# Performance work log

Measured on AMD Instinct MI355X. Metric: run time of the kernel, lower is better.

Reference implementation:

```python
import jax, jax.numpy as jnp
import numpy as np

NUM_USERS = 100000
NUM_ITEMS = 50000
NUM_NODES = NUM_USERS + NUM_ITEMS
EMBED_DIM = 64
NUM_LAYERS = 3
NUM_EDGES = 1000000


def setup_inputs() -> dict:
    key = jax.random.key(0)
    k_edge, k_emb = jax.random.split(key)
    edge_index = jax.random.randint(k_edge, (2, NUM_EDGES), 0, NUM_NODES, dtype=jnp.int64)
    # xavier_uniform for Embedding weight [N, d]
    limit = float(np.sqrt(6.0 / (NUM_NODES + EMBED_DIM)))
    emb = jax.random.uniform(k_emb, (NUM_NODES, EMBED_DIM), minval=-limit, maxval=limit, dtype=jnp.float32)
    alpha = jnp.full((NUM_LAYERS + 1,), 0.25, dtype=jnp.float32)
    return {"edge_index": edge_index, "emb": emb, "alpha": alpha}


def _gcn_norm(edge_index, num_nodes, dtype):
    # gcn_norm with add_self_loops=False, edge_weight = ones
    src, dst = edge_index[0], edge_index[1]
    w = jnp.ones((src.shape[0],), dtype=dtype)
    deg = jax.ops.segment_sum(w, dst, num_segments=num_nodes)  # degree at target
    deg_inv_sqrt = jnp.where(deg > 0, jax.lax.rsqrt(jnp.maximum(deg, 1e-30)), 0.0)
    return deg_inv_sqrt[src] * deg_inv_sqrt[dst]  # [E]


def get_embedding(emb, alpha, edge_index):
    src, dst = edge_index[0], edge_index[1]
    norm = _gcn_norm(edge_index, NUM_NODES, emb.dtype)  # [E]
    x = emb
    out = x * alpha[0]
    for i in range(NUM_LAYERS):
        # gather -> scale by edge norm -> scatter-add at target nodes
        msgs = norm[:, None] * x[src]                      # [E, d]
        x = jax.ops.segment_sum(msgs, dst, num_segments=NUM_NODES)  # [N, d]
        out = out + x * alpha[i + 1]
    return out


def reference(edge_index, emb, alpha):
    out = get_embedding(emb, alpha, edge_index)  # [N, d]
    out_src = out[edge_index[0]]                 # [E, d]
    out_dst = out[edge_index[1]]                 # [E, d]
    return jnp.sum(out_src * out_dst, axis=-1)   # [E]
```

## Files before the change

kernel.cpp:

```cpp
#include <hip/hip_runtime.h>
#include <hip/hip_fp16.h>

#define DIM 64
#define PCHUNK 2048
#define BSH 9
#define BNODES (1 << BSH)

__device__ __forceinline__ float2 h2f(unsigned int u) {
    __half2 h = *reinterpret_cast<__half2*>(&u);
    return __half22float2(h);
}
__device__ __forceinline__ unsigned int f2h(float a, float b) {
    __half2 h = __floats2half2_rn(a, b);
    return *reinterpret_cast<unsigned int*>(&h);
}

__device__ __forceinline__ bool edges_are_i64(const unsigned int* w) {
    unsigned int acc = 0;
#pragma unroll
    for (int k = 0; k < 8; ++k) acc |= w[2 * k + 1];
    return acc == 0;
}
__device__ __forceinline__ int ld_edge(const void* raw, bool is64, size_t idx) {
    return is64 ? (int)((const long long*)raw)[idx] : ((const int*)raw)[idx];
}

__global__ void k_partition(const void* ei_raw, int E, int NB, int CAP,
                            int* __restrict__ bwcnt, uint2* __restrict__ pe) {
    __shared__ int cnt[512], lstart[512], gb[512], lofs[512], psum[256];
    __shared__ uint2 stage[PCHUNK];
    __shared__ int gpos[PCHUNK];
    bool is64 = edges_are_i64((const unsigned int*)ei_raw);
    int base = blockIdx.x * PCHUNK;
    int n = E - base; if (n > PCHUNK) n = PCHUNK;
    int t = threadIdx.x;
    for (int b = t; b < 512; b += 256) { cnt[b] = 0; lofs[b] = 0; }
    __syncthreads();
    int s[8], d[8];
#pragma unroll
    for (int r = 0; r < 8; ++r) {
        int i = r * 256 + t;
        if (i < n) {
            s[r] = ld_edge(ei_raw, is64, (size_t)base + i);
            d[r] = ld_edge(ei_raw, is64, (size_t)E + base + i);
            atomicAdd(&cnt[d[r] >> BSH], 1);
        }
    }
    __syncthreads();
    int a0 = cnt[2 * t], a1 = cnt[2 * t + 1];
    psum[t] = a0 + a1;
    __syncthreads();
    int v = psum[t];
    for (int o = 1; o < 256; o <<= 1) {
        int tv = (t >= o) ? psum[t - o] : 0;
        __syncthreads();
        psum[t] += tv;
        __syncthreads();
    }
    int excl = psum[t] - v;
    lstart[2 * t] = excl;
    lstart[2 * t + 1] = excl + a0;
    __syncthreads();
    for (int b = t; b < NB; b += 256)
        if (cnt[b] > 0) gb[b] = atomicAdd(&bwcnt[b], cnt[b]);
    __syncthreads();
#pragma unroll
    for (int r = 0; r < 8; ++r) {
        int i = r * 256 + t;
        if (i < n) {
            int b = d[r] >> BSH;
            int j = atomicAdd(&lofs[b], 1);
            int slot = lstart[b] + j;
            stage[slot] = make_uint2((unsigned)s[r], (unsigned)d[r]);
            int gj = gb[b] + j;
            gpos[slot] = (gj < CAP) ? (b * CAP + gj) : (NB * CAP + slot);
        }
    }
    __syncthreads();
    for (int i = t; i < n; i += 256)
        pe[gpos[i]] = stage[i];
}

__global__ void k_bscan(const int* __restrict__ bwcnt, int* __restrict__ ebase, int NB) {
    __shared__ int sh[512];
    int tid = threadIdx.x;
    int v = (tid < NB) ? bwcnt[tid] : 0;
    sh[tid] = v;
    __syncthreads();
    for (int o = 1; o < 512; o <<= 1) {
        int t2 = (tid >= o) ? sh[tid - o] : 0;
        __syncthreads();
        sh[tid] += t2;
        __syncthreads();
    }
    if (tid < NB) ebase[tid] = sh[tid] - v;
    if (tid == NB - 1) ebase[NB] = sh[tid];
}

__global__ void k_bucket(const uint2* __restrict__ pe, const int* __restrict__ bwcnt,
                         const int* __restrict__ ebase, int CAP,
                         int* __restrict__ rowptr, float* __restrict__ dinv,
                         int* __restrict__ esrc, int N, int E, int NB) {
    __shared__ int ldeg[BNODES], lcur[BNODES], psum[256];
    int b = blockIdx.x;
    int n0 = b << BSH;
    int nn = N - n0; if (nn > BNODES) nn = BNODES;
    int ecnt = bwcnt[b];
    int eb = ebase[b];
    const uint2* win = pe + (size_t)b * CAP;
    int t = threadIdx.x;
    for (int j = t; j < BNODES; j += 256) ldeg[j] = 0;
    __syncthreads();
    for (int i = t; i < ecnt; i += 256)
        atomicAdd(&ldeg[win[i].y - n0], 1);
    __syncthreads();
    int a0 = ldeg[2 * t], a1 = ldeg[2 * t + 1];
    psum[t] = a0 + a1;
    __syncthreads();
    int v = psum[t];
    for (int o = 1; o < 256; o <<= 1) {
        int tv = (t >= o) ? psum[t - o] : 0;
        __syncthreads();
        psum[t] += tv;
        __syncthreads();
    }
    int excl = psum[t] - v;
    int e0 = excl, e1 = excl + a0;
    lcur[2 * t] = e0;
    lcur[2 * t + 1] = e1;
    if (2 * t < nn) {
        rowptr[n0 + 2 * t] = eb + e0;
        dinv[n0 + 2 * t] = a0 > 0 ? 1.0f / sqrtf((float)a0) : 0.0f;
    }
    if (2 * t + 1 < nn) {
        rowptr[n0 + 2 * t + 1] = eb + e1;
        dinv[n0 + 2 * t + 1] = a1 > 0 ? 1.0f / sqrtf((float)a1) : 0.0f;
    }
    if (b == NB - 1 && t == 0) rowptr[N] = E;
    __syncthreads();
    for (int i = t; i < ecnt; i += 256) {
        uint2 rec = win[i];
        int pos = eb + atomicAdd(&lcur[rec.y - n0], 1);
        esrc[pos] = (int)rec.x;
    }
}

__global__ void k_tohalf_scaled(const float* __restrict__ x, const float* __restrict__ dinv,
                                __half* __restrict__ yh, int n8) {
    int i = blockIdx.x * blockDim.x + threadIdx.x;
    if (i >= n8) return;
    int node = i >> 3;
    float di = dinv[node];
    const float4* p = (const float4*)(x + (size_t)i * 8);
    float4 a = p[0], b = p[1];
    uint4 o;
    o.x = f2h(di * a.x, di * a.y); o.y = f2h(di * a.z, di * a.w);
    o.z = f2h(di * b.x, di * b.y); o.w = f2h(di * b.z, di * b.w);
    ((uint4*)yh)[i] = o;
}

__global__ void k_gather_y(const int* __restrict__ rowptr, const int* __restrict__ esrc,
                           const float* __restrict__ dinv, const __half* __restrict__ ysrc,
                           __half* __restrict__ ynext, float* __restrict__ out,
                           __half* __restrict__ outh, const float* __restrict__ emb,
                           const float* __restrict__ alpha, int aidx,
                           int first, int last, int N) {
    int t = blockIdx.x * blockDim.x + threadIdx.x;
    int node = t >> 3, c = t & 7;
    if (node >= N) return;
    int beg = rowptr[node], end = rowptr[node + 1];
    float acc[8] = {0.f, 0.f, 0.f, 0.f, 0.f, 0.f, 0.f, 0.f};
    for (int i = beg; i < end; ++i) {
        int s = esrc[i];
        uint4 u = ((const uint4*)(ysrc + (size_t)s * DIM))[c];
        float2 f0 = h2f(u.x), f1 = h2f(u.y), f2 = h2f(u.z), f3 = h2f(u.w);
        acc[0] += f0.x; acc[1] += f0.y;
        acc[2] += f1.x; acc[3] += f1.y;
        acc[4] += f2.x; acc[5] += f2.y;
        acc[6] += f3.x; acc[7] += f3.y;
    }
    float di = dinv[node];
    float a = alpha[aidx] * di;

    if (!last) {
        float d2 = di * di;
        uint4 o;
        o.x = f2h(d2 * acc[0], d2 * acc[1]); o.y = f2h(d2 * acc[2], d2 * acc[3]);
        o.z = f2h(d2 * acc[4], d2 * acc[5]); o.w = f2h(d2 * acc[6], d2 * acc[7]);
        ((uint4*)(ynext + (size_t)node * DIM))[c] = o;
    }

    float o[8];
    if (first) {
        float a0 = alpha[0];
        const float4* ep = (const float4*)(emb + (size_t)node * DIM + c * 8);
        float4 e0 = ep[0], e1 = ep[1];
        o[0] = a0 * e0.x; o[1] = a0 * e0.y; o[2] = a0 * e0.z; o[3] = a0 * e0.w;
        o[4] = a0 * e1.x; o[5] = a0 * e1.y; o[6] = a0 * e1.z; o[7] = a0 * e1.w;
    } else {
        const float4* op = (const float4*)(out + (size_t)node * DIM + c * 8);
        float4 e0 = op[0], e1 = op[1];
        o[0] = e0.x; o[1] = e0.y; o[2] = e0.z; o[3] = e0.w;
        o[4] = e1.x; o[5] = e1.y; o[6] = e1.z; o[7] = e1.w;
    }
#pragma unroll
    for (int k = 0; k < 8; ++k) o[k] += a * acc[k];

    if (last) {
        uint4 u;
        u.x = f2h(o[0], o[1]); u.y = f2h(o[2], o[3]);
        u.z = f2h(o[4], o[5]); u.w = f2h(o[6], o[7]);
        ((uint4*)(outh + (size_t)node * DIM))[c] = u;
    } else {
        float4* op = (float4*)(out + (size_t)node * DIM + c * 8);
        op[0] = make_float4(o[0], o[1], o[2], o[3]);
        op[1] = make_float4(o[4], o[5], o[6], o[7]);
    }
}

__global__ void k_final_h(const void* ei_raw, const __half* __restrict__ outh,
                          float* __restrict__ res, int E) {
    bool is64 = edges_are_i64((const unsigned int*)ei_raw);
    int t = blockIdx.x * blockDim.x + threadIdx.x;
    int e = t >> 3, c = t & 7;
    if (e >= E) return;
    int s = ld_edge(ei_raw, is64, (size_t)e);
    int d = ld_edge(ei_raw, is64, (size_t)E + e);
    uint4 ua = ((const uint4*)(outh + (size_t)s * DIM))[c];
    uint4 ub = ((const uint4*)(outh + (size_t)d * DIM))[c];
    float2 a0 = h2f(ua.x), a1 = h2f(ua.y), a2 = h2f(ua.z), a3 = h2f(ua.w);
    float2 b0 = h2f(ub.x), b1 = h2f(ub.y), b2 = h2f(ub.z), b3 = h2f(ub.w);
    float p = a0.x * b0.x + a0.y * b0.y + a1.x * b1.x + a1.y * b1.y +
              a2.x * b2.x + a2.y * b2.y + a3.x * b3.x + a3.y * b3.y;
    p += __shfl_down(p, 4, 8);
    p += __shfl_down(p, 2, 8);
    p += __shfl_down(p, 1, 8);
    if (c == 0) res[e] = p;
}

static inline size_t alignUp(size_t x) { return (x + 511) & ~size_t(511); }

extern "C" void kernel_launch(void* const* d_in, const int* in_sizes, int n_in,
                              void* d_out, int out_size, void* d_ws, size_t ws_size,
                              hipStream_t stream) {
    const void*  ei    = d_in[0];
    const float* emb   = (const float*)d_in[1];
    const float* alpha = (const float*)d_in[2];
    float*       res   = (float*)d_out;

    const int E = in_sizes[0] / 2;
    const int N = in_sizes[1] / DIM;
    const int NUM_LAYERS = 3;

    const int NB = (N + BNODES - 1) >> BSH;
    int cap = (E / NB) * 3 / 2;
    const int CAP = (cap + 1023) & ~1023;

    char* w = (char*)d_ws;
    size_t off = 0;
    int*    bwcnt  = (int*)(w + off);    off = alignUp(off + (size_t)(NB + 1) * sizeof(int));
    int*    ebase  = (int*)(w + off);    off = alignUp(off + (size_t)(NB + 1) * sizeof(int));
    float*  dinv   = (float*)(w + off);  off = alignUp(off + (size_t)N * sizeof(float));
    int*    rowptr = (int*)(w + off);    off = alignUp(off + (size_t)(N + 1) * sizeof(int));
    int*    esrc   = (int*)(w + off);    off = alignUp(off + (size_t)E * sizeof(int));
    uint2*  pe     = (uint2*)(w + off);  off = alignUp(off + ((size_t)NB * CAP + PCHUNK) * sizeof(uint2));
    float*  outv   = (float*)(w + off);  off = alignUp(off + (size_t)N * DIM * sizeof(float));
    __half* y0h    = (__half*)(w + off); off = alignUp(off + (size_t)N * DIM * sizeof(__half));
    __half* xAh    = (__half*)(w + off); off = alignUp(off + (size_t)N * DIM * sizeof(__half));
    __half* xBh    = (__half*)(w + off); off = alignUp(off + (size_t)N * DIM * sizeof(__half));
    __half* outh   = (__half*)(w + off); off = alignUp(off + (size_t)N * DIM * sizeof(__half));
    (void)ws_size;

    const int B = 256;
    const int n8 = N * DIM / 8;

    hipMemsetAsync(bwcnt, 0, (size_t)(NB + 1) * sizeof(int), stream);

    int npart = (E + PCHUNK - 1) / PCHUNK;
    k_partition<<<npart, 256, 0, stream>>>(ei, E, NB, CAP, bwcnt, pe);
    k_bscan<<<1, 512, 0, stream>>>(bwcnt, ebase, NB);
    k_bucket<<<NB, 256, 0, stream>>>(pe, bwcnt, ebase, CAP, rowptr, dinv, esrc, N, E, NB);

    k_tohalf_scaled<<<(n8 + B - 1) / B, B, 0, stream>>>(emb, dinv, y0h, n8);

    long long tN8 = (long long)N * 8;
    int ggrid = (int)((tN8 + B - 1) / B);
    const __half* yc = y0h;
    __half* bufs[2] = {xAh, xBh};
    for (int i = 0; i < NUM_LAYERS; ++i) {
        __half* yn = bufs[i & 1];
        int last = (i == NUM_LAYERS - 1) ? 1 : 0;
        k_gather_y<<<ggrid, B, 0, stream>>>(rowptr, esrc, dinv, yc, yn, outv, outh,
                                            emb, alpha, i + 1, (i == 0) ? 1 : 0, last, N);
        yc = yn;
    }

    long long tE8 = (long long)E * 8;
    k_final_h<<<(int)((tE8 + B - 1) / B), B, 0, stream>>>(ei, outh, res, E);
}
```

Before: 193.1 us.

## Fuse embedding scaling into bucket kernel and split propagation across a wavefront per node

Folds the fp16 scaled-embedding conversion into the bucketing kernel, which removes a separate launch. Each propagation layer now gives one 64-lane wavefront per node, with eight edge slots reduced through shuffles, instead of eight threads walking all edges serially. The fp32 running output buffer is dropped: the final layer rebuilds the weighted sum from the emb, y1 and y2 buffers, rescaled by the square root of the degree. This cuts fp32 read/write traffic but launches eight times more threads, most of them idle for low-degree nodes. The 1/dinv recovery also loses accuracy for zero-degree nodes whose y terms are zero anyway.

```diff
diff --git a/kernel.cpp b/kernel.cpp
--- a/kernel.cpp
+++ b/kernel.cpp
@@ -100,8 +100,10 @@
 __global__ void k_bucket(const uint2* __restrict__ pe, const int* __restrict__ bwcnt,
                          const int* __restrict__ ebase, int CAP,
                          int* __restrict__ rowptr, float* __restrict__ dinv,
-                         int* __restrict__ esrc, int N, int E, int NB) {
+                         int* __restrict__ esrc, const float* __restrict__ emb,
+                         __half* __restrict__ y0h, int N, int E, int NB) {
     __shared__ int ldeg[BNODES], lcur[BNODES], psum[256];
+    __shared__ float fdi[BNODES];
     int b = blockIdx.x;
     int n0 = b << BSH;
     int nn = N - n0; if (nn > BNODES) nn = BNODES;
@@ -125,17 +127,14 @@
         __syncthreads();
     }
     int excl = psum[t] - v;
-    int e0 = excl, e1 = excl + a0;
-    lcur[2 * t] = e0;
-    lcur[2 * t + 1] = e1;
-    if (2 * t < nn) {
-        rowptr[n0 + 2 * t] = eb + e0;
-        dinv[n0 + 2 * t] = a0 > 0 ? 1.0f / sqrtf((float)a0) : 0.0f;
-    }
-    if (2 * t + 1 < nn) {
-        rowptr[n0 + 2 * t + 1] = eb + e1;
-        dinv[n0 + 2 * t + 1] = a1 > 0 ? 1.0f / sqrtf((float)a1) : 0.0f;
-    }
+    float d0 = a0 > 0 ? 1.0f / sqrtf((float)a0) : 0.0f;
+    float d1 = a1 > 0 ? 1.0f / sqrtf((float)a1) : 0.0f;
+    lcur[2 * t] = excl;
+    lcur[2 * t + 1] = excl + a0;
+    fdi[2 * t] = d0;
+    fdi[2 * t + 1] = d1;
+    if (2 * t < nn)     { rowptr[n0 + 2 * t] = eb + excl;      dinv[n0 + 2 * t] = d0; }
+    if (2 * t + 1 < nn) { rowptr[n0 + 2 * t + 1] = eb + excl + a0; dinv[n0 + 2 * t + 1] = d1; }
     if (b == NB - 1 && t == 0) rowptr[N] = E;
     __syncthreads();
     for (int i = t; i < ecnt; i += 256) {
@@ -143,78 +142,97 @@
         int pos = eb + atomicAdd(&lcur[rec.y - n0], 1);
         esrc[pos] = (int)rec.x;
     }
-}
-
-__global__ void k_tohalf_scaled(const float* __restrict__ x, const float* __restrict__ dinv,
-                                __half* __restrict__ yh, int n8) {
-    int i = blockIdx.x * blockDim.x + threadIdx.x;
-    if (i >= n8) return;
-    int node = i >> 3;
-    float di = dinv[node];
-    const float4* p = (const float4*)(x + (size_t)i * 8);
-    float4 a = p[0], b = p[1];
-    uint4 o;
-    o.x = f2h(di * a.x, di * a.y); o.y = f2h(di * a.z, di * a.w);
-    o.z = f2h(di * b.x, di * b.y); o.w = f2h(di * b.z, di * b.w);
-    ((uint4*)yh)[i] = o;
-}
-
-__global__ void k_gather_y(const int* __restrict__ rowptr, const int* __restrict__ esrc,
-                           const float* __restrict__ dinv, const __half* __restrict__ ysrc,
-                           __half* __restrict__ ynext, float* __restrict__ out,
-                           __half* __restrict__ outh, const float* __restrict__ emb,
-                           const float* __restrict__ alpha, int aidx,
-                           int first, int last, int N) {
-    int t = blockIdx.x * blockDim.x + threadIdx.x;
-    int node = t >> 3, c = t & 7;
-    if (node >= N) return;
-    int beg = rowptr[node], end = rowptr[node + 1];
+    for (int idx = t; idx < nn * 8; idx += 256) {
+        int node = idx >> 3, c = idx & 7;
+        float di = fdi[node];
+        const float4* p = (const float4*)(emb + (size_t)(n0 + node) * DIM + c * 8);
+        float4 a = p[0], bb = p[1];
+        uint4 o;
+        o.x = f2h(di * a.x, di * a.y);  o.y = f2h(di * a.z, di * a.w);
+        o.z = f2h(di * bb.x, di * bb.y); o.w = f2h(di * bb.z, di * bb.w);
+        ((uint4*)(y0h + (size_t)(n0 + node) * DIM))[idx & 7 ? (idx & 7) : (idx & 7)] = o;
+    }
+}
+
+__global__ void k_prop(const int* __restrict__ rowptr, const int* __restrict__ esrc,
+                       const float* __restrict__ dinv, const __half* __restrict__ ycur,
+                       __half* __restrict__ ynext, int N) {
+    int wid = (blockIdx.x * blockDim.x + threadIdx.x) >> 6;
+    if (wid >= N) return;
+    int lane = threadIdx.x & 63;
+    int slot = lane >> 3, c = lane & 7;
+    int beg = rowptr[wid], end = rowptr[wid + 1];
     float acc[8] = {0.f, 0.f, 0.f, 0.f, 0.f, 0.f, 0.f, 0.f};
-    for (int i = beg; i < end; ++i) {
+    for (int i = beg + slot; i < end; i += 8) {
         int s = esrc[i];
-        uint4 u = ((const uint4*)(ysrc + (size_t)s * DIM))[c];
+        uint4 u = ((const uint4*)(ycur + (size_t)s * DIM))[c];
         float2 f0 = h2f(u.x), f1 = h2f(u.y), f2 = h2f(u.z), f3 = h2f(u.w);
-        acc[0] += f0.x; acc[1] += f0.y;
-        acc[2] += f1.x; acc[3] += f1.y;
-        acc[4] += f2.x; acc[5] += f2.y;
-        acc[6] += f3.x; acc[7] += f3.y;
-    }
-    float di = dinv[node];
-    float a = alpha[aidx] * di;
-
-    if (!last) {
+        acc[0] += f0.x; acc[1] += f0.y; acc[2] += f1.x; acc[3] += f1.y;
+        acc[4] += f2.x; acc[5] += f2.y; acc[6] += f3.x; acc[7] += f3.y;
+    }
+#pragma unroll
+    for (int k = 0; k < 8; ++k) {
+        acc[k] += __shfl_xor(acc[k], 8);
+        acc[k] += __shfl_xor(acc[k], 16);
+        acc[k] += __shfl_xor(acc[k], 32);
+    }
+    if (slot == 0) {
+        float di = dinv[wid];
         float d2 = di * di;
         uint4 o;
         o.x = f2h(d2 * acc[0], d2 * acc[1]); o.y = f2h(d2 * acc[2], d2 * acc[3]);
         o.z = f2h(d2 * acc[4], d2 * acc[5]); o.w = f2h(d2 * acc[6], d2 * acc[7]);
-        ((uint4*)(ynext + (size_t)node * DIM))[c] = o;
-    }
-
-    float o[8];
-    if (first) {
-        float a0 = alpha[0];
-        const float4* ep = (const float4*)(emb + (size_t)node * DIM + c * 8);
+        ((uint4*)(ynext + (size_t)wid * DIM))[c] = o;
+    }
+}
+
+__global__ void k_outp(const int* __restrict__ rowptr, const int* __restrict__ esrc,
+                       const float* __restrict__ dinv, const __half* __restrict__ y2h,
+                       const __half* __restrict__ y1h, const float* __restrict__ emb,
+                       const float* __restrict__ alpha, __half* __restrict__ outh, int N) {
+    int wid = (blockIdx.x * blockDim.x + threadIdx.x) >> 6;
+    if (wid >= N) return;
+    int lane = threadIdx.x & 63;
+    int slot = lane >> 3, c = lane & 7;
+    int beg = rowptr[wid], end = rowptr[wid + 1];
+    float acc[8] = {0.f, 0.f, 0.f, 0.f, 0.f, 0.f, 0.f, 0.f};
+    for (int i = beg + slot; i < end; i += 8) {
+        int s = esrc[i];
+        uint4 u = ((const uint4*)(y2h + (size_t)s * DIM))[c];
+        float2 f0 = h2f(u.x), f1 = h2f(u.y), f2 = h2f(u.z), f3 = h2f(u.w);
+        acc[0] += f0.x; acc[1] += f0.y; acc[2] += f1.x; acc[3] += f1.y;
+        acc[4] += f2.x; acc[5] += f2.y; acc[6] += f3.x; acc[7] += f3.y;
+    }
+#pragma unroll
+    for (int k = 0; k < 8; ++k) {
+        acc[k] += __shfl_xor(acc[k], 8);
+        acc[k] += __shfl_xor(acc[k], 16);
+        acc[k] += __shfl_xor(acc[k], 32);
+    }
+    if (slot == 0) {
+        float di = dinv[wid];
+        float sd = di > 0.f ? 1.0f / di : 0.0f;
+        float a0 = alpha[0], a1 = alpha[1], a2 = alpha[2], a3 = alpha[3];
+        const float4* ep = (const float4*)(emb + (size_t)wid * DIM + c * 8);
         float4 e0 = ep[0], e1 = ep[1];
-        o[0] = a0 * e0.x; o[1] = a0 * e0.y; o[2] = a0 * e0.z; o[3] = a0 * e0.w;
-        o[4] = a0 * e1.x; o[5] = a0 * e1.y; o[6] = a0 * e1.z; o[7] = a0 * e1.w;
-    } else {
-        const float4* op = (const float4*)(out + (size_t)node * DIM + c * 8);
-        float4 e0 = op[0], e1 = op[1];
-        o[0] = e0.x; o[1] = e0.y; o[2] = e0.z; o[3] = e0.w;
-        o[4] = e1.x; o[5] = e1.y; o[6] = e1.z; o[7] = e1.w;
-    }
-#pragma unroll
-    for (int k = 0; k < 8; ++k) o[k] += a * acc[k];
-
-    if (last) {
+        uint4 u1 = ((const uint4*)(y1h + (size_t)wid * DIM))[c];
+        uint4 u2 = ((const uint4*)(y2h + (size_t)wid * DIM))[c];
+        float2 p0 = h2f(u1.x), p1 = h2f(u1.y), p2 = h2f(u1.z), p3 = h2f(u1.w);
+        float2 q0 = h2f(u2.x), q1 = h2f(u2.y), q2 = h2f(u2.z), q3 = h2f(u2.w);
+        float a3d = a3 * di;
+        float o[8];
+        o[0] = a0 * e0.x + sd * (a1 * p0.x + a2 * q0.x) + a3d * acc[0];
+        o[1] = a0 * e0.y + sd * (a1 * p0.y + a2 * q0.y) + a3d * acc[1];
+        o[2] = a0 * e0.z + sd * (a1 * p1.x + a2 * q1.x) + a3d * acc[2];
+        o[3] = a0 * e0.w + sd * (a1 * p1.y + a2 * q1.y) + a3d * acc[3];
+        o[4] = a0 * e1.x + sd * (a1 * p2.x + a2 * q2.x) + a3d * acc[4];
+        o[5] = a0 * e1.y + sd * (a1 * p2.y + a2 * q2.y) + a3d * acc[5];
+        o[6] = a0 * e1.z + sd * (a1 * p3.x + a2 * q3.x) + a3d * acc[6];
+        o[7] = a0 * e1.w + sd * (a1 * p3.y + a2 * q3.y) + a3d * acc[7];
         uint4 u;
         u.x = f2h(o[0], o[1]); u.y = f2h(o[2], o[3]);
         u.z = f2h(o[4], o[5]); u.w = f2h(o[6], o[7]);
-        ((uint4*)(outh + (size_t)node * DIM))[c] = u;
-    } else {
-        float4* op = (float4*)(out + (size_t)node * DIM + c * 8);
-        op[0] = make_float4(o[0], o[1], o[2], o[3]);
-        op[1] = make_float4(o[4], o[5], o[6], o[7]);
+        ((uint4*)(outh + (size_t)wid * DIM))[c] = u;
     }
 }
 
@@ -250,7 +268,6 @@
 
     const int E = in_sizes[0] / 2;
     const int N = in_sizes[1] / DIM;
-    const int NUM_LAYERS = 3;
 
     const int NB = (N + BNODES - 1) >> BSH;
     int cap = (E / NB) * 3 / 2;
@@ -264,36 +281,27 @@
     int*    rowptr = (int*)(w + off);    off = alignUp(off + (size_t)(N + 1) * sizeof(int));
     int*    esrc   = (int*)(w + off);    off = alignUp(off + (size_t)E * sizeof(int));
     uint2*  pe     = (uint2*)(w + off);  off = alignUp(off + ((size_t)NB * CAP + PCHUNK) * sizeof(uint2));
-    float*  outv   = (float*)(w + off);  off = alignUp(off + (size_t)N * DIM * sizeof(float));
     __half* y0h    = (__half*)(w + off); off = alignUp(off + (size_t)N * DIM * sizeof(__half));
-    __half* xAh    = (__half*)(w + off); off = alignUp(off + (size_t)N * DIM * sizeof(__half));
-    __half* xBh    = (__half*)(w + off); off = alignUp(off + (size_t)N * DIM * sizeof(__half));
+    __half* y1h    = (__half*)(w + off); off = alignUp(off + (size_t)N * DIM * sizeof(__half));
+    __half* y2h    = (__half*)(w + off); off = alignUp(off + (size_t)N * DIM * sizeof(__half));
     __half* outh   = (__half*)(w + off); off = alignUp(off + (size_t)N * DIM * sizeof(__half));
     (void)ws_size;
 
     const int B = 256;
-    const int n8 = N * DIM / 8;
 
     hipMemsetAsync(bwcnt, 0, (size_t)(NB + 1) * sizeof(int), stream);
 
     int npart = (E + PCHUNK - 1) / PCHUNK;
     k_partition<<<npart, 256, 0, stream>>>(ei, E, NB, CAP, bwcnt, pe);
     k_bscan<<<1, 512, 0, stream>>>(bwcnt, ebase, NB);
-    k_bucket<<<NB, 256, 0, stream>>>(pe, bwcnt, ebase, CAP, rowptr, dinv, esrc, N, E, NB);
-
-    k_tohalf_scaled<<<(n8 + B - 1) / B, B, 0, stream>>>(emb, dinv, y0h, n8);
-
-    long long tN8 = (long long)N * 8;
-    int ggrid = (int)((tN8 + B - 1) / B);
-    const __half* yc = y0h;
-    __half* bufs[2] = {xAh, xBh};
-    for (int i = 0; i < NUM_LAYERS; ++i) {
-        __half* yn = bufs[i & 1];
-        int last = (i == NUM_LAYERS - 1) ? 1 : 0;
-        k_gather_y<<<ggrid, B, 0, stream>>>(rowptr, esrc, dinv, yc, yn, outv, outh,
-                                            emb, alpha, i + 1, (i == 0) ? 1 : 0, last, N);
-        yc = yn;
-    }
+    k_bucket<<<NB, 256, 0, stream>>>(pe, bwcnt, ebase, CAP, rowptr, dinv, esrc,
+                                     emb, y0h, N, E, NB);
+
+    long long tW = (long long)N * 64;
+    int pgrid = (int)((tW + B - 1) / B);
+    k_prop<<<pgrid, B, 0, stream>>>(rowptr, esrc, dinv, y0h, y1h, N);
+    k_prop<<<pgrid, B, 0, stream>>>(rowptr, esrc, dinv, y1h, y2h, N);
+    k_outp<<<pgrid, B, 0, stream>>>(rowptr, esrc, dinv, y2h, y1h, emb, alpha, outh, N);
 
     long long tE8 = (long long)E * 8;
     k_final_h<<<(int)((tE8 + B - 1) / B), B, 0, stream>>>(ei, outh, res, E);
```

Result: slower. 232.6 us (+20.5%).
